# Kernel optimization log

Measured on AMD Instinct MI355X. Metric: run time of the kernel, lower is better.

Reference implementation:

```python
import jax, jax.numpy as jnp
import numpy as np

N_R = 20          # cfg['n_r']
H = 0.01          # cfg['h'] integration step
ALPHA_N = 0.1     # alpha(D_s_n, R_s_n) folded scale (stable: |eig(H*matAn)| << 2.8)
ALPHA_P = 0.08    # alpha(D_s_p, R_s_p)
BETA_N = -0.5     # -beta(...) for negative electrode
BETA_P = 0.4      # beta(...) for positive electrode


def _make_mats():
    n = N_R - 1
    # FDM tridiagonal (1,-2,1) radial diffusion stencil (spm_model.matA)
    matA = (jnp.diag(-2.0 * jnp.ones(n))
            + jnp.diag(jnp.ones(n - 1), 1)
            + jnp.diag(jnp.ones(n - 1), -1)).astype(jnp.float32)
    # boundary-flux input vector (spm_model.matB): only surface node driven
    matB = jnp.zeros(n, jnp.float32).at[-1].set(1.0)
    matAn = ALPHA_N * matA
    matBn = ALPHA_N * BETA_N * matB
    matAp = ALPHA_P * matA
    matBp = ALPHA_P * BETA_P * matB
    return matAn, matBn, matAp, matBp


def setup_inputs() -> dict:
    key = jax.random.key(0)
    k1, k2 = jax.random.split(key)
    n = N_R - 1
    B, K = 4096, 1024
    x = jax.random.normal(k1, (B, 2 * n), jnp.float32)
    i_seq = jax.random.normal(k2, (B, K), jnp.float32)
    matAn, matBn, matAp, matBp = _make_mats()
    return {"x": x, "i_seq": i_seq,
            "matAn": matAn, "matBn": matBn,
            "matAp": matAp, "matBp": matBp,
            "k": K}


def _rk4_step(x, i_col, A, Bv):
    # f(x) = A @ x + B * i  (batched: x [B,n], i_col [B,1], Bv [n])
    def f(y):
        return y @ A.T + i_col * Bv
    k1 = f(x)
    k2 = f(x + 0.5 * H * k1)
    k3 = f(x + 0.5 * H * k2)
    k4 = f(x + H * k3)
    return x + (H / 6.0) * (k1 + 2.0 * k2 + 2.0 * k3 + k4)


def reference(x, i_seq, matAn, matBn, matAp, matBp, k):
    n = N_R - 1
    xn0, xp0 = x[:, :n], x[:, n:]

    def step(carry, i_t):
        xn, xp = carry
        i_col = i_t[:, None]                      # [B,1]
        xn = _rk4_step(xn, i_col, matAn, matBn)
        xp = _rk4_step(xp, i_col, matAp, matBp)
        return (xn, xp), jnp.concatenate([xn, xp], axis=1)  # [B, 2n]

    _, x_all = jax.lax.scan(step, (xn0, xp0), i_seq.T)      # [k, B, 2n]
    return jnp.transpose(x_all, (1, 2, 0))                  # [B, 2n, k]
```

## Files before the change

kernel.cpp:

```cpp
#include <hip/hip_runtime.h>

#define NCOMP 19
#define NB    4096
#define PI_F  3.14159265358979323846f

typedef float f32x4 __attribute__((ext_vector_type(4)));

__device__ __forceinline__ constexpr float vconst(int k, int j) {
  constexpr float S[21] = {
    0.0f, 0.15643446504023087f, 0.3090169943749474f, 0.45399049973954675f,
    0.5877852522924731f, 0.7071067811865476f, 0.8090169943749475f,
    0.8910065241883679f, 0.9510565162951535f, 0.9876883405951378f, 1.0f,
    0.9876883405951378f, 0.9510565162951535f, 0.8910065241883679f,
    0.8090169943749475f, 0.7071067811865476f, 0.5877852522924731f,
    0.45399049973954675f, 0.3090169943749474f, 0.15643446504023087f, 0.0f};
  int m = ((k + 1) * (j + 1)) % 40;
  float s = (m <= 20) ? S[m] : -S[m - 20];
  return s * 0.31622776601683794f;
}

template <int CTRL, int RMASK>
__device__ __forceinline__ float dpp_add(float x) {
  int v = __builtin_amdgcn_update_dpp(0, __float_as_int(x), CTRL, RMASK, 0xf, true);
  return x + __int_as_float(v);
}
__device__ __forceinline__ float wave_iscan(float x) {
  x = dpp_add<0x111, 0xf>(x);
  x = dpp_add<0x112, 0xf>(x);
  x = dpp_add<0x114, 0xf>(x);
  x = dpp_add<0x118, 0xf>(x);
  x = dpp_add<0x142, 0xa>(x);
  x = dpp_add<0x143, 0xc>(x);
  return x;
}

__global__ __launch_bounds__(256) void spm_fused(
    const float* __restrict__ xin, const float* __restrict__ iseq,
    const float* __restrict__ An, const float* __restrict__ Bn,
    const float* __restrict__ Ap, const float* __restrict__ Bp,
    float* __restrict__ out)
{
  __shared__ float xs0[NCOMP];
  __shared__ float4 mcv[NCOMP];
  __shared__ float2 mgw[NCOMP];
  __shared__ __align__(16) float wtot[NCOMP][4];

  const int t = threadIdx.x;
  const int lane = t & 63, wid = t >> 6;
  const int b = blockIdx.x >> 1, sys = blockIdx.x & 1;
  const float alpha = sys ? Ap[1] : An[1];
  const float ha    = 0.01f * alpha;

  if (t < NCOMP) xs0[t] = xin[(size_t)b * (2 * NCOMP) + sys * NCOMP + t];
  __syncthreads();

  if (t < NCOMP) {
    float ab = sys ? Bp[NCOMP - 1] : Bn[NCOMP - 1];
    float sk = sinf((float)(t + 1) * (PI_F / 40.0f));
    float z  = ha * (-4.0f * sk * sk);
    float g  = 1.0f + z * (1.0f + z * (0.5f + z * ((1.0f/6.0f) + z * (1.0f/24.0f))));
    float S  = 1.0f + z * (0.5f + z * ((1.0f/6.0f) + z * (1.0f/24.0f)));
    float gi = 1.0f / g;
    float vlast = sinf((float)(((t + 1) * NCOMP) % 40) * (PI_F / 20.0f)) *
                  0.31622776601683794f;
    float w = 0.01f * S * ab * vlast;
    float s0 = 0.0f;
#pragma unroll
    for (int j = 0; j < NCOMP; ++j)
      s0 = fmaf(sinf((float)(((t + 1) * (j + 1)) % 40) * (PI_F / 20.0f)) *
                    0.31622776601683794f, xs0[j], s0);
    mcv[t] = make_float4(gi, w * gi, __builtin_log2f(g), s0);
    mgw[t] = make_float2(g, w);
  }
  __syncthreads();

  const float4 iv = *reinterpret_cast<const float4*>(iseq + (size_t)b * 1024 + t * 4);
  const float pos = (float)(4 * t);

  float Cp[NCOMP];
#pragma unroll
  for (int k = 0; k < NCOMP; ++k) {
    const float4 c = mcv[k];
    float r = iv.x + c.x * (iv.y + c.x * (iv.z + c.x * iv.w));
    float a = __builtin_exp2f(-pos * c.z) * r;
    float v = wave_iscan(a);
    if (lane == 63) wtot[k][wid] = v;
    Cp[k] = v - a;
  }
  __syncthreads();

  float sA[NCOMP], sB[NCOMP], sC[NCOMP], sD[NCOMP];
#pragma unroll
  for (int k = 0; k < NCOMP; ++k) {
    const float4 c = mcv[k];
    const float2 gw = mgw[k];
    float4 q = *reinterpret_cast<const float4*>(&wtot[k][0]);
    float C = Cp[k];
    if (wid > 0) C += q.x;
    if (wid > 1) C += q.y;
    if (wid > 2) C += q.z;
    float s = __builtin_exp2f(pos * c.z) * fmaf(c.y, C, c.w);
    sA[k] = fmaf(gw.x, s,     gw.y * iv.x);
    sB[k] = fmaf(gw.x, sA[k], gw.y * iv.y);
    sC[k] = fmaf(gw.x, sB[k], gw.y * iv.z);
    sD[k] = fmaf(gw.x, sC[k], gw.y * iv.w);
  }

  float* orow = out + ((size_t)b * (2 * NCOMP) + sys * NCOMP) * 1024 + t * 4;
#pragma unroll
  for (int jj = 0; jj < 9; ++jj) {
    float E0 = 0.f, E1 = 0.f, E2 = 0.f, E3 = 0.f;
    float O0 = 0.f, O1 = 0.f, O2 = 0.f, O3 = 0.f;
#pragma unroll
    for (int k = 0; k < NCOMP; k += 2) {
      const float vk = vconst(k, jj);
      E0 = fmaf(sA[k], vk, E0); E1 = fmaf(sB[k], vk, E1);
      E2 = fmaf(sC[k], vk, E2); E3 = fmaf(sD[k], vk, E3);
    }
#pragma unroll
    for (int k = 1; k < NCOMP; k += 2) {
      const float vk = vconst(k, jj);
      O0 = fmaf(sA[k], vk, O0); O1 = fmaf(sB[k], vk, O1);
      O2 = fmaf(sC[k], vk, O2); O3 = fmaf(sD[k], vk, O3);
    }
    f32x4 vp = { E0 + O0, E1 + O1, E2 + O2, E3 + O3 };
    f32x4 vm = { E0 - O0, E1 - O1, E2 - O2, E3 - O3 };
    __builtin_nontemporal_store(vp, reinterpret_cast<f32x4*>(orow + (size_t)jj * 1024));
    __builtin_nontemporal_store(vm, reinterpret_cast<f32x4*>(orow + (size_t)(18 - jj) * 1024));
  }
  {
    float E0 = 0.f, E1 = 0.f, E2 = 0.f, E3 = 0.f;
#pragma unroll
    for (int k = 0; k < NCOMP; k += 2) {
      const float vk = vconst(k, 9);
      E0 = fmaf(sA[k], vk, E0); E1 = fmaf(sB[k], vk, E1);
      E2 = fmaf(sC[k], vk, E2); E3 = fmaf(sD[k], vk, E3);
    }
    f32x4 vc = { E0, E1, E2, E3 };
    __builtin_nontemporal_store(vc, reinterpret_cast<f32x4*>(orow + (size_t)9 * 1024));
  }
}

extern "C" void kernel_launch(void* const* d_in, const int* in_sizes, int n_in,
                              void* d_out, int out_size, void* d_ws, size_t ws_size,
                              hipStream_t stream) {
  const float* x    = (const float*)d_in[0];
  const float* iseq = (const float*)d_in[1];
  const float* An   = (const float*)d_in[2];
  const float* Bn   = (const float*)d_in[3];
  const float* Ap   = (const float*)d_in[4];
  const float* Bp   = (const float*)d_in[5];
  float* out = (float*)d_out;

  spm_fused<<<NB * 2, 256, 0, stream>>>(x, iseq, An, Bn, Ap, Bp, out);
}
```

Measured before the change: 149.0 us.

## Precompute eigen tables, issue iseq load early, use packed FMA and batched stores

Replaces the per-block sinf evaluations in the setup phase with a compile-time constant-memory table of eigenvector entries and eigenvalues. The iseq load is moved ahead of the first barrier so its latency overlaps the setup. The output transform now keeps its state as float2 pairs so packed FMA instructions can be used, and all 19 output rows are gathered in registers before being stored together. This is meant to cut setup ALU work and the VALU cost of the projection, though holding every output row at once raises register pressure. The kernel stays memory-bound on its large output write, so the gain may be limited.

```diff
diff --git a/kernel.cpp b/kernel.cpp
--- a/kernel.cpp
+++ b/kernel.cpp
@@ -2,22 +2,35 @@
 
 #define NCOMP 19
 #define NB    4096
-#define PI_F  3.14159265358979323846f
 
+typedef float f32x2 __attribute__((ext_vector_type(2)));
 typedef float f32x4 __attribute__((ext_vector_type(4)));
 
-__device__ __forceinline__ constexpr float vconst(int k, int j) {
-  constexpr float S[21] = {
-    0.0f, 0.15643446504023087f, 0.3090169943749474f, 0.45399049973954675f,
-    0.5877852522924731f, 0.7071067811865476f, 0.8090169943749475f,
-    0.8910065241883679f, 0.9510565162951535f, 0.9876883405951378f, 1.0f,
-    0.9876883405951378f, 0.9510565162951535f, 0.8910065241883679f,
-    0.8090169943749475f, 0.7071067811865476f, 0.5877852522924731f,
-    0.45399049973954675f, 0.3090169943749474f, 0.15643446504023087f, 0.0f};
-  int m = ((k + 1) * (j + 1)) % 40;
-  float s = (m <= 20) ? S[m] : -S[m - 20];
-  return s * 0.31622776601683794f;
+constexpr float S20[21] = {
+  0.0f, 0.15643446504023087f, 0.3090169943749474f, 0.45399049973954675f,
+  0.5877852522924731f, 0.7071067811865476f, 0.8090169943749475f,
+  0.8910065241883679f, 0.9510565162951535f, 0.9876883405951378f, 1.0f,
+  0.9876883405951378f, 0.9510565162951535f, 0.8910065241883679f,
+  0.8090169943749475f, 0.7071067811865476f, 0.5877852522924731f,
+  0.45399049973954675f, 0.3090169943749474f, 0.15643446504023087f, 0.0f};
+
+__host__ __device__ constexpr float sval(int m) {
+  return (m <= 20) ? S20[m] : -S20[m - 20];
 }
+__host__ __device__ constexpr float vconst(int k, int j) {
+  return sval(((k + 1) * (j + 1)) % 40) * 0.31622776601683794f;
+}
+
+struct Tabs { float v[NCOMP][NCOMP]; float lam[NCOMP]; };
+__host__ __device__ constexpr Tabs make_tabs() {
+  Tabs T{};
+  for (int k = 0; k < NCOMP; ++k) {
+    for (int j = 0; j < NCOMP; ++j) T.v[k][j] = vconst(k, j);
+    T.lam[k] = -2.0f * (1.0f - sval((k + 11) % 40));
+  }
+  return T;
+}
+__constant__ Tabs VT = make_tabs();
 
 template <int CTRL, int RMASK>
 __device__ __forceinline__ float dpp_add(float x) {
@@ -51,30 +64,26 @@
   const float alpha = sys ? Ap[1] : An[1];
   const float ha    = 0.01f * alpha;
 
+  const float4 iv = *reinterpret_cast<const float4*>(iseq + (size_t)b * 1024 + t * 4);
+
   if (t < NCOMP) xs0[t] = xin[(size_t)b * (2 * NCOMP) + sys * NCOMP + t];
   __syncthreads();
 
   if (t < NCOMP) {
     float ab = sys ? Bp[NCOMP - 1] : Bn[NCOMP - 1];
-    float sk = sinf((float)(t + 1) * (PI_F / 40.0f));
-    float z  = ha * (-4.0f * sk * sk);
+    float z  = ha * VT.lam[t];
     float g  = 1.0f + z * (1.0f + z * (0.5f + z * ((1.0f/6.0f) + z * (1.0f/24.0f))));
     float S  = 1.0f + z * (0.5f + z * ((1.0f/6.0f) + z * (1.0f/24.0f)));
     float gi = 1.0f / g;
-    float vlast = sinf((float)(((t + 1) * NCOMP) % 40) * (PI_F / 20.0f)) *
-                  0.31622776601683794f;
-    float w = 0.01f * S * ab * vlast;
+    float w  = 0.01f * S * ab * VT.v[t][NCOMP - 1];
     float s0 = 0.0f;
 #pragma unroll
-    for (int j = 0; j < NCOMP; ++j)
-      s0 = fmaf(sinf((float)(((t + 1) * (j + 1)) % 40) * (PI_F / 20.0f)) *
-                    0.31622776601683794f, xs0[j], s0);
+    for (int j = 0; j < NCOMP; ++j) s0 = fmaf(VT.v[t][j], xs0[j], s0);
     mcv[t] = make_float4(gi, w * gi, __builtin_log2f(g), s0);
     mgw[t] = make_float2(g, w);
   }
   __syncthreads();
 
-  const float4 iv = *reinterpret_cast<const float4*>(iseq + (size_t)b * 1024 + t * 4);
   const float pos = (float)(4 * t);
 
   float Cp[NCOMP];
@@ -89,7 +98,7 @@
   }
   __syncthreads();
 
-  float sA[NCOMP], sB[NCOMP], sC[NCOMP], sD[NCOMP];
+  f32x2 s01[NCOMP], s23[NCOMP];
 #pragma unroll
   for (int k = 0; k < NCOMP; ++k) {
     const float4 c = mcv[k];
@@ -99,46 +108,52 @@
     if (wid > 0) C += q.x;
     if (wid > 1) C += q.y;
     if (wid > 2) C += q.z;
-    float s = __builtin_exp2f(pos * c.z) * fmaf(c.y, C, c.w);
-    sA[k] = fmaf(gw.x, s,     gw.y * iv.x);
-    sB[k] = fmaf(gw.x, sA[k], gw.y * iv.y);
-    sC[k] = fmaf(gw.x, sB[k], gw.y * iv.z);
-    sD[k] = fmaf(gw.x, sC[k], gw.y * iv.w);
+    float s  = __builtin_exp2f(pos * c.z) * fmaf(c.y, C, c.w);
+    float sA = fmaf(gw.x, s,  gw.y * iv.x);
+    float sB = fmaf(gw.x, sA, gw.y * iv.y);
+    float sC = fmaf(gw.x, sB, gw.y * iv.z);
+    float sD = fmaf(gw.x, sC, gw.y * iv.w);
+    s01[k] = (f32x2){sA, sB};
+    s23[k] = (f32x2){sC, sD};
+  }
+
+  f32x4 ob[NCOMP];
+#pragma unroll
+  for (int jj = 0; jj < 9; ++jj) {
+    f32x2 E01 = {0.f, 0.f}, E23 = {0.f, 0.f};
+    f32x2 O01 = {0.f, 0.f}, O23 = {0.f, 0.f};
+#pragma unroll
+    for (int k = 0; k < NCOMP; k += 2) {
+      const f32x2 vk = { vconst(k, jj), vconst(k, jj) };
+      E01 = __builtin_elementwise_fma(s01[k], vk, E01);
+      E23 = __builtin_elementwise_fma(s23[k], vk, E23);
+    }
+#pragma unroll
+    for (int k = 1; k < NCOMP; k += 2) {
+      const f32x2 vk = { vconst(k, jj), vconst(k, jj) };
+      O01 = __builtin_elementwise_fma(s01[k], vk, O01);
+      O23 = __builtin_elementwise_fma(s23[k], vk, O23);
+    }
+    f32x2 p01 = E01 + O01, p23 = E23 + O23;
+    f32x2 m01 = E01 - O01, m23 = E23 - O23;
+    ob[jj]      = (f32x4){p01.x, p01.y, p23.x, p23.y};
+    ob[18 - jj] = (f32x4){m01.x, m01.y, m23.x, m23.y};
+  }
+  {
+    f32x2 E01 = {0.f, 0.f}, E23 = {0.f, 0.f};
+#pragma unroll
+    for (int k = 0; k < NCOMP; k += 2) {
+      const f32x2 vk = { vconst(k, 9), vconst(k, 9) };
+      E01 = __builtin_elementwise_fma(s01[k], vk, E01);
+      E23 = __builtin_elementwise_fma(s23[k], vk, E23);
+    }
+    ob[9] = (f32x4){E01.x, E01.y, E23.x, E23.y};
   }
 
   float* orow = out + ((size_t)b * (2 * NCOMP) + sys * NCOMP) * 1024 + t * 4;
 #pragma unroll
-  for (int jj = 0; jj < 9; ++jj) {
-    float E0 = 0.f, E1 = 0.f, E2 = 0.f, E3 = 0.f;
-    float O0 = 0.f, O1 = 0.f, O2 = 0.f, O3 = 0.f;
-#pragma unroll
-    for (int k = 0; k < NCOMP; k += 2) {
-      const float vk = vconst(k, jj);
-      E0 = fmaf(sA[k], vk, E0); E1 = fmaf(sB[k], vk, E1);
-      E2 = fmaf(sC[k], vk, E2); E3 = fmaf(sD[k], vk, E3);
-    }
-#pragma unroll
-    for (int k = 1; k < NCOMP; k += 2) {
-      const float vk = vconst(k, jj);
-      O0 = fmaf(sA[k], vk, O0); O1 = fmaf(sB[k], vk, O1);
-      O2 = fmaf(sC[k], vk, O2); O3 = fmaf(sD[k], vk, O3);
-    }
-    f32x4 vp = { E0 + O0, E1 + O1, E2 + O2, E3 + O3 };
-    f32x4 vm = { E0 - O0, E1 - O1, E2 - O2, E3 - O3 };
-    __builtin_nontemporal_store(vp, reinterpret_cast<f32x4*>(orow + (size_t)jj * 1024));
-    __builtin_nontemporal_store(vm, reinterpret_cast<f32x4*>(orow + (size_t)(18 - jj) * 1024));
-  }
-  {
-    float E0 = 0.f, E1 = 0.f, E2 = 0.f, E3 = 0.f;
-#pragma unroll
-    for (int k = 0; k < NCOMP; k += 2) {
-      const float vk = vconst(k, 9);
-      E0 = fmaf(sA[k], vk, E0); E1 = fmaf(sB[k], vk, E1);
-      E2 = fmaf(sC[k], vk, E2); E3 = fmaf(sD[k], vk, E3);
-    }
-    f32x4 vc = { E0, E1, E2, E3 };
-    __builtin_nontemporal_store(vc, reinterpret_cast<f32x4*>(orow + (size_t)9 * 1024));
-  }
+  for (int j = 0; j < NCOMP; ++j)
+    __builtin_nontemporal_store(ob[j], reinterpret_cast<f32x4*>(orow + (size_t)j * 1024));
 }
 
 extern "C" void kernel_launch(void* const* d_in, const int* in_sizes, int n_in,
```

Result: faster. 127.9 us, median of 2 (-14.2%).
